# Kernel optimization log

Hardware: AMD Instinct MI355X
Metric: run time of the kernel (lower is better)

Reference implementation:

```python
import jax, jax.numpy as jnp
import numpy as np

H = 64  # LSTM hidden size ('unit' in the torch module)

def _lstm_params(k, scale):
    k1, k2, k3 = jax.random.split(k, 3)
    wih = jax.random.uniform(k1, (4 * H, 1), minval=-scale, maxval=scale, dtype=jnp.float32)
    whh = jax.random.uniform(k2, (4 * H, H), minval=-scale, maxval=scale, dtype=jnp.float32)
    b = jax.random.uniform(k3, (4 * H,), minval=-scale, maxval=scale, dtype=jnp.float32)  # b_ih + b_hh folded
    return wih, whh, b

def _linear_params(k, out_d, in_d):
    k1, k2 = jax.random.split(k)
    s = 1.0 / np.sqrt(in_d)
    w = jax.random.uniform(k1, (out_d, in_d), minval=-s, maxval=s, dtype=jnp.float32)
    b = jax.random.uniform(k2, (out_d,), minval=-s, maxval=s, dtype=jnp.float32)
    return w, b

def setup_inputs():
    key = jax.random.key(0)
    ks = jax.random.split(key, 16)
    B, T, A = 4096, 32, 6
    s = 1.0 / np.sqrt(H)
    inp = {
        'x0': jax.random.normal(ks[0], (B, T, 1), dtype=jnp.float32),
        'x1': jax.random.normal(ks[1], (B, T, 1), dtype=jnp.float32),
        'x2': jax.random.normal(ks[2], (B, T, 1), dtype=jnp.float32),
        's2': jax.random.normal(ks[3], (B, 3), dtype=jnp.float32),
    }
    for name, k in [('q00', ks[4]), ('q01', ks[5]), ('i00', ks[6]), ('i01', ks[7]), ('i02', ks[8])]:
        wih, whh, b = _lstm_params(k, s)
        inp[name + '_wih'], inp[name + '_whh'], inp[name + '_b'] = wih, whh, b
    inp['q03_w'], inp['q03_b'] = _linear_params(ks[9], H, 3)
    inp['q1_w'], inp['q1_b'] = _linear_params(ks[10], H, 4 * H)
    inp['q2_w'], inp['q2_b'] = _linear_params(ks[11], A, H)
    inp['i03_w'], inp['i03_b'] = _linear_params(ks[12], H, 3)
    inp['i1_w'], inp['i1_b'] = _linear_params(ks[13], H, 4 * H)
    inp['i2_w'], inp['i2_b'] = _linear_params(ks[14], A, H)
    return inp

def _lstm_hn(x, wih, whh, b):
    # x: [B,T,1] -> final hidden state h_T: [B,H]. PyTorch gate order: i, f, g, o.
    B = x.shape[0]
    gx = jnp.einsum('bti,gi->btg', x, wih) + b        # [B,T,4H], input part precomputed
    gx = jnp.swapaxes(gx, 0, 1)                        # [T,B,4H]
    h0 = jnp.zeros((B, H), x.dtype)
    def step(carry, g):
        h, c = carry
        g = g + h @ whh.T
        i, f, gg, o = jnp.split(g, 4, axis=-1)
        c = jax.nn.sigmoid(f) * c + jax.nn.sigmoid(i) * jnp.tanh(gg)
        h = jax.nn.sigmoid(o) * jnp.tanh(c)
        return (h, c), None
    (h, _), _ = jax.lax.scan(step, (h0, h0), gx)
    return h

def reference(x0, x1, x2, s2,
              q00_wih, q00_whh, q00_b, q01_wih, q01_whh, q01_b,
              i00_wih, i00_whh, i00_b, i01_wih, i01_whh, i01_b, i02_wih, i02_whh, i02_b,
              q03_w, q03_b, q1_w, q1_b, q2_w, q2_b,
              i03_w, i03_b, i1_w, i1_b, i2_w, i2_b):
    # q branch (NOTE: original code applies q01 to BOTH x1 and x2 -- reproduced faithfully)
    hn0 = _lstm_hn(x0, q00_wih, q00_whh, q00_b)
    hn1 = _lstm_hn(x1, q01_wih, q01_whh, q01_b)
    hn2 = _lstm_hn(x2, q01_wih, q01_whh, q01_b)
    hn3 = jax.nn.relu(s2 @ q03_w.T + q03_b)
    hq = jnp.concatenate([hn0, hn1, hn2, hn3], axis=1)  # [B,4H]
    q = jax.nn.relu(hq @ q1_w.T + q1_b)
    # i branch
    hn0 = _lstm_hn(x0, i00_wih, i00_whh, i00_b)
    hn1 = _lstm_hn(x1, i01_wih, i01_whh, i01_b)
    hn2 = _lstm_hn(x2, i02_wih, i02_whh, i02_b)
    hn3 = jax.nn.relu(s2 @ i03_w.T + i03_b)
    hi = jnp.concatenate([hn0, hn1, hn2, hn3], axis=1)
    i = jax.nn.relu(hi @ i1_w.T + i1_b)
    i = jax.nn.relu(i @ i2_w.T + i2_b)                   # [B,A]
    return (q @ q2_w.T + q2_b, jax.nn.log_softmax(i, axis=1), i)
```

## Files before the change

kernel.cpp:

```cpp
#include <hip/hip_runtime.h>

#define BTOT 4096
#define TS 32

typedef __attribute__((ext_vector_type(8))) short bfrag;
typedef __attribute__((ext_vector_type(4))) float f32x4;

#define S1 (-1.44269504089f)
#define S2 (-2.88539008178f)

__device__ __forceinline__ short f2bf(float f){
  union { float f; unsigned u; } v; v.f = f;
  unsigned r = v.u + 0x7FFFu + ((v.u >> 16) & 1u);
  return (short)(r >> 16);
}
__device__ __forceinline__ float bf2f(short s){
  union { unsigned u; float f; } v; v.u = ((unsigned)(unsigned short)s) << 16; return v.f;
}
__device__ __forceinline__ f32x4 exp2v(f32x4 a){
  f32x4 r;
  r[0] = __builtin_amdgcn_exp2f(a[0]);
  r[1] = __builtin_amdgcn_exp2f(a[1]);
  r[2] = __builtin_amdgcn_exp2f(a[2]);
  r[3] = __builtin_amdgcn_exp2f(a[3]);
  return r;
}
__device__ __forceinline__ f32x4 rcpv(f32x4 a){
  f32x4 r;
  r[0] = __builtin_amdgcn_rcpf(a[0]);
  r[1] = __builtin_amdgcn_rcpf(a[1]);
  r[2] = __builtin_amdgcn_rcpf(a[2]);
  r[3] = __builtin_amdgcn_rcpf(a[3]);
  return r;
}

struct LstmP {
  const float* x[6];
  const float* wih[6];
  const float* whh[6];
  const float* bias[6];
  float* hout;
};

struct EpiP {
  const float* hout;
  const float* s2;
  const float* w03[2]; const float* b03[2];
  const float* w1[2];  const float* b1[2];
  const float* w2[2];  const float* b2[2];
  float* out;
};

__global__ __launch_bounds__(256, 3) void lstm6(LstmP p){
  const int run = blockIdx.y;
  const int b0 = blockIdx.x * 32;
  const int t = threadIdx.x;
  const int w = t >> 6, lane = t & 63;
  const int i16 = lane & 15, q = lane >> 4;

  __shared__ bfrag hb[2][2][16*9];
  __shared__ float xsT[TS*36];

  const float* __restrict__ whh = p.whh[run];

  bfrag B[4][2];
  float wihv[4], bv[4];
#pragma unroll
  for (int g = 0; g < 4; ++g){
    const float sg = (g == 2) ? S2 : S1;
    const int n = 64*g + 16*w + i16;
    const float* wr = whh + n*64;
#pragma unroll
    for (int kf = 0; kf < 2; ++kf){
      const float* src = wr + 32*kf + 8*q;
      bfrag bb;
#pragma unroll
      for (int j = 0; j < 8; ++j) bb[j] = f2bf(src[j] * sg);
      B[g][kf] = bb;
    }
    wihv[g] = p.wih[run][n] * sg;
    bv[g]   = p.bias[run][n] * sg;
  }
  {
    const float* x = p.x[run] + (size_t)b0 * TS;
    for (int i = t; i < 32*TS; i += 256){
      int m = i >> 5, s = i & 31;
      xsT[s*36 + m] = x[i];
    }
    int* hz = (int*)&hb[0][0][0];
    for (int i = t; i < 1152; i += 256) hz[i] = 0;
  }
  __syncthreads();

  f32x4 c4[2];
  c4[0] = (f32x4){0.f,0.f,0.f,0.f};
  c4[1] = (f32x4){0.f,0.f,0.f,0.f};

  const int af = i16*9 + q;
  for (int s = 0; s < TS; ++s){
#pragma unroll
    for (int tile = 0; tile < 2; ++tile){
      const bfrag* hh = hb[s & 1][tile];
      short* wh = (short*)hb[(s+1) & 1][tile];
      bfrag ah0 = hh[af];
      bfrag ah1 = hh[af + 4];
      f32x4 xm4 = *(const f32x4*)(xsT + s*36 + 16*tile + 4*q);

      f32x4 acc[4];
#pragma unroll
      for (int g = 0; g < 4; ++g){
        acc[g] = xm4 * wihv[g] + bv[g];
        acc[g] = __builtin_amdgcn_mfma_f32_16x16x32_bf16(ah0, B[g][0], acc[g], 0,0,0);
        acc[g] = __builtin_amdgcn_mfma_f32_16x16x32_bf16(ah1, B[g][1], acc[g], 0,0,0);
      }
      f32x4 ei = exp2v(acc[0]);
      f32x4 ef = exp2v(acc[1]);
      f32x4 eg = exp2v(acc[2]);
      f32x4 eo = exp2v(acc[3]);
      f32x4 pf = 1.0f + ef;
      f32x4 D1 = (1.0f + eg) * (1.0f + ei);
      f32x4 num = __builtin_elementwise_fma(c4[tile], D1, (1.0f - eg) * pf);
      f32x4 cc = num * rcpv(pf * D1);
      c4[tile] = cc;
      f32x4 ec = exp2v(cc * S2);
      f32x4 hv = (1.0f - ec) * rcpv((1.0f + ec) * (1.0f + eo));
      if (s == TS-1){
#pragma unroll
        for (int r = 0; r < 4; ++r)
          p.hout[((size_t)run*BTOT + b0 + 16*tile + 4*q + r)*64 + 16*w + i16] = hv[r];
      } else {
        const int wbase = (4*q)*72 + 16*w + i16;
#pragma unroll
        for (int r = 0; r < 4; ++r)
          wh[wbase + r*72] = f2bf(hv[r]);
      }
    }
    __syncthreads();
  }
}

__global__ __launch_bounds__(256) void epilogue(EpiP p){
  const int br = blockIdx.y;
  const int b0 = blockIdx.x * 16;
  const int t = threadIdx.x;
  const int wave = t >> 6, lane = t & 63;
  const int i16 = lane & 15, q = lane >> 4;

  __shared__ bfrag hqv_hi[16*33], hqv_lo[16*33];
  __shared__ float qv[16*66];
  __shared__ float iv[16][6];

  const float* hbase = p.hout + (size_t)br*3*BTOT*64;
  {
    short4* dh = (short4*)hqv_hi;
    short4* dl = (short4*)hqv_lo;
    for (int i = t; i < 768; i += 256){
      int run = i >> 8, ii = i & 255;
      int e = ii >> 4, j4 = ii & 15;
      float4 v = *(const float4*)(hbase + ((size_t)run*BTOT + b0 + e)*64 + j4*4);
      short4 h, l;
      short x0 = f2bf(v.x); h.x = x0; l.x = f2bf(v.x - bf2f(x0));
      short x1 = f2bf(v.y); h.y = x1; l.y = f2bf(v.y - bf2f(x1));
      short x2 = f2bf(v.z); h.z = x2; l.z = f2bf(v.z - bf2f(x2));
      short x3 = f2bf(v.w); h.w = x3; l.w = f2bf(v.w - bf2f(x3));
      int o4 = e*66 + run*16 + j4;
      dh[o4] = h;
      dl[o4] = l;
    }
  }
  {
    short* sh = (short*)hqv_hi;
    short* sl = (short*)hqv_lo;
    const float* w03 = p.w03[br];
    const float* b03 = p.b03[br];
    for (int i = t; i < 1024; i += 256){
      int e = i >> 6, jj = i & 63;
      const float* s2r = p.s2 + (size_t)(b0 + e)*3;
      float v = fmaf(s2r[0], w03[jj*3+0],
                fmaf(s2r[1], w03[jj*3+1],
                fmaf(s2r[2], w03[jj*3+2], b03[jj])));
      v = fmaxf(v, 0.0f);
      int off = e*264 + 192 + jj;
      short hi = f2bf(v);
      sh[off] = hi;
      sl[off] = f2bf(v - bf2f(hi));
    }
  }
  __syncthreads();

  {
    const int n = 16*wave + i16;
    const float* w1r = p.w1[br] + (size_t)n*256;
    f32x4 acc;
    { float bb = p.b1[br][n]; acc[0]=bb; acc[1]=bb; acc[2]=bb; acc[3]=bb; }
#pragma unroll
    for (int ks = 0; ks < 8; ++ks){
      bfrag ah = hqv_hi[i16*33 + 4*ks + q];
      bfrag al = hqv_lo[i16*33 + 4*ks + q];
      const float* src = w1r + 32*ks + 8*q;
      bfrag bh, bl;
#pragma unroll
      for (int j = 0; j < 8; ++j){
        float f = src[j];
        short hi = f2bf(f);
        bh[j] = hi;
        bl[j] = f2bf(f - bf2f(hi));
      }
      acc = __builtin_amdgcn_mfma_f32_16x16x32_bf16(ah, bh, acc, 0,0,0);
      acc = __builtin_amdgcn_mfma_f32_16x16x32_bf16(al, bh, acc, 0,0,0);
      acc = __builtin_amdgcn_mfma_f32_16x16x32_bf16(ah, bl, acc, 0,0,0);
    }
#pragma unroll
    for (int r = 0; r < 4; ++r)
      qv[(4*q + r)*66 + n] = fmaxf(acc[r], 0.0f);
  }
  __syncthreads();

  if (t < 96){
    int e = t / 6, a = t % 6;
    const float* w2r = p.w2[br] + a*64;
    const float* qe = qv + e*66;
    float acc2 = p.b2[br][a];
#pragma unroll 8
    for (int k = 0; k < 64; ++k) acc2 = fmaf(qe[k], w2r[k], acc2);
    int b = b0 + e;
    if (br == 0){
      p.out[(size_t)b*6 + a] = acc2;
    } else {
      float v = fmaxf(acc2, 0.0f);
      iv[e][a] = v;
      p.out[(size_t)2*BTOT*6 + (size_t)b*6 + a] = v;
    }
  }
  __syncthreads();
  if (br == 1 && t < 16){
    float m = iv[t][0];
    for (int a2 = 1; a2 < 6; ++a2) m = fmaxf(m, iv[t][a2]);
    float ss = 0.0f;
    for (int a2 = 0; a2 < 6; ++a2) ss += __expf(iv[t][a2] - m);
    float ls = __logf(ss);
    int b = b0 + t;
    for (int a2 = 0; a2 < 6; ++a2)
      p.out[(size_t)BTOT*6 + (size_t)b*6 + a2] = iv[t][a2] - m - ls;
  }
}

extern "C" void kernel_launch(void* const* d_in, const int* in_sizes, int n_in,
                              void* d_out, int out_size, void* d_ws, size_t ws_size,
                              hipStream_t stream) {
  const float* x0 = (const float*)d_in[0];
  const float* x1 = (const float*)d_in[1];
  const float* x2 = (const float*)d_in[2];
  const float* s2 = (const float*)d_in[3];

  LstmP lp;
  lp.x[0]=x0; lp.x[1]=x1; lp.x[2]=x2; lp.x[3]=x0; lp.x[4]=x1; lp.x[5]=x2;
  const int wbase[6] = {4, 7, 7, 10, 13, 16};
  for (int r = 0; r < 6; ++r){
    lp.wih[r]  = (const float*)d_in[wbase[r]+0];
    lp.whh[r]  = (const float*)d_in[wbase[r]+1];
    lp.bias[r] = (const float*)d_in[wbase[r]+2];
  }
  lp.hout = (float*)d_ws;

  lstm6<<<dim3(BTOT/32, 6), 256, 0, stream>>>(lp);

  EpiP ep;
  ep.hout = (const float*)d_ws;
  ep.s2 = s2;
  ep.w03[0]=(const float*)d_in[19]; ep.b03[0]=(const float*)d_in[20];
  ep.w1 [0]=(const float*)d_in[21]; ep.b1 [0]=(const float*)d_in[22];
  ep.w2 [0]=(const float*)d_in[23]; ep.b2 [0]=(const float*)d_in[24];
  ep.w03[1]=(const float*)d_in[25]; ep.b03[1]=(const float*)d_in[26];
  ep.w1 [1]=(const float*)d_in[27]; ep.b1 [1]=(const float*)d_in[28];
  ep.w2 [1]=(const float*)d_in[29]; ep.b2 [1]=(const float*)d_in[30];
  ep.out = (float*)d_out;

  epilogue<<<dim3(BTOT/16, 2), 256, 0, stream>>>(ep);
}
```

Baseline: 184.5 us.

## Repartition LSTM blocks to two runs per block with 16-row batch tiles

Each block now processes two LSTM runs over 16 batch rows instead of one run over 32 rows. Each wave owns 32 hidden columns (two column groups) rather than 16, so every wave holds twice the recurrent weight fragments in registers. Input weights and biases move from registers into shared memory. The grid changes from 128x6 to 256x3 blocks, giving more independent blocks with shorter per-block work. In exchange, register pressure rises from the doubled B fragments, which may hurt occupancy under launch_bounds(256,3).

```diff
diff --git a/kernel.cpp b/kernel.cpp
--- a/kernel.cpp
+++ b/kernel.cpp
@@ -52,45 +52,61 @@
 };
 
 __global__ __launch_bounds__(256, 3) void lstm6(LstmP p){
-  const int run = blockIdx.y;
-  const int b0 = blockIdx.x * 32;
+  const int z = blockIdx.y;
+  const int b0 = blockIdx.x * 16;
   const int t = threadIdx.x;
-  const int w = t >> 6, lane = t & 63;
+  const int ww = t >> 6, lane = t & 63;
+  const int rl = ww >> 1, half = ww & 1;
+  const int run = 2*z + rl;
   const int i16 = lane & 15, q = lane >> 4;
 
   __shared__ bfrag hb[2][2][16*9];
-  __shared__ float xsT[TS*36];
+  __shared__ float xsT[2][TS*20];
+  __shared__ __align__(16) float wb[4][16][20];
 
   const float* __restrict__ whh = p.whh[run];
 
-  bfrag B[4][2];
-  float wihv[4], bv[4];
+  bfrag B[4][2][2];
 #pragma unroll
   for (int g = 0; g < 4; ++g){
     const float sg = (g == 2) ? S2 : S1;
-    const int n = 64*g + 16*w + i16;
-    const float* wr = whh + n*64;
-#pragma unroll
-    for (int kf = 0; kf < 2; ++kf){
-      const float* src = wr + 32*kf + 8*q;
-      bfrag bb;
-#pragma unroll
-      for (int j = 0; j < 8; ++j) bb[j] = f2bf(src[j] * sg);
-      B[g][kf] = bb;
-    }
-    wihv[g] = p.wih[run][n] * sg;
-    bv[g]   = p.bias[run][n] * sg;
-  }
-  {
+#pragma unroll
+    for (int cg = 0; cg < 2; ++cg){
+      const int n = 64*g + 32*half + 16*cg + i16;
+      const float* wr = whh + n*64;
+#pragma unroll
+      for (int kf = 0; kf < 2; ++kf){
+        const float* src = wr + 32*kf + 8*q;
+        bfrag bb;
+#pragma unroll
+        for (int j = 0; j < 8; ++j) bb[j] = f2bf(src[j] * sg);
+        B[g][cg][kf] = bb;
+      }
+      if (q == 0){
+        wb[ww][i16][cg*8 + g]     = p.wih[run][n] * sg;
+        wb[ww][i16][cg*8 + 4 + g] = p.bias[run][n] * sg;
+      }
+    }
+  }
+
+  if (half == 0){
     const float* x = p.x[run] + (size_t)b0 * TS;
-    for (int i = t; i < 32*TS; i += 256){
+    for (int i = lane; i < 16*TS; i += 64){
       int m = i >> 5, s = i & 31;
-      xsT[s*36 + m] = x[i];
-    }
+      xsT[rl][s*20 + m] = x[i];
+    }
+  }
+  {
     int* hz = (int*)&hb[0][0][0];
-    for (int i = t; i < 1152; i += 256) hz[i] = 0;
-  }
-  __syncthreads();
+    for (int i = t; i < 1152; i += 256){
+      int lr = i / 576, rem = i - lr*576;
+      hz[lr*1152 + rem] = 0;
+    }
+  }
+  __syncthreads();
+
+  const float* xp = xsT[rl];
+  const float* wbp = &wb[ww][i16][0];
 
   f32x4 c4[2];
   c4[0] = (f32x4){0.f,0.f,0.f,0.f};
@@ -98,20 +114,22 @@
 
   const int af = i16*9 + q;
   for (int s = 0; s < TS; ++s){
-#pragma unroll
-    for (int tile = 0; tile < 2; ++tile){
-      const bfrag* hh = hb[s & 1][tile];
-      short* wh = (short*)hb[(s+1) & 1][tile];
-      bfrag ah0 = hh[af];
-      bfrag ah1 = hh[af + 4];
-      f32x4 xm4 = *(const f32x4*)(xsT + s*36 + 16*tile + 4*q);
-
+    const bfrag* hh = hb[rl][s & 1];
+    short* wh = (short*)&hb[rl][(s+1) & 1][0];
+    bfrag ah0 = hh[af];
+    bfrag ah1 = hh[af + 4];
+    f32x4 xm4 = *(const f32x4*)(xp + s*20 + 4*q);
+
+#pragma unroll
+    for (int cg = 0; cg < 2; ++cg){
+      f32x4 wv = *(const f32x4*)(wbp + cg*8);
+      f32x4 bb = *(const f32x4*)(wbp + cg*8 + 4);
       f32x4 acc[4];
 #pragma unroll
       for (int g = 0; g < 4; ++g){
-        acc[g] = xm4 * wihv[g] + bv[g];
-        acc[g] = __builtin_amdgcn_mfma_f32_16x16x32_bf16(ah0, B[g][0], acc[g], 0,0,0);
-        acc[g] = __builtin_amdgcn_mfma_f32_16x16x32_bf16(ah1, B[g][1], acc[g], 0,0,0);
+        acc[g] = xm4 * wv[g] + bb[g];
+        acc[g] = __builtin_amdgcn_mfma_f32_16x16x32_bf16(ah0, B[g][cg][0], acc[g], 0,0,0);
+        acc[g] = __builtin_amdgcn_mfma_f32_16x16x32_bf16(ah1, B[g][cg][1], acc[g], 0,0,0);
       }
       f32x4 ei = exp2v(acc[0]);
       f32x4 ef = exp2v(acc[1]);
@@ -119,20 +137,20 @@
       f32x4 eo = exp2v(acc[3]);
       f32x4 pf = 1.0f + ef;
       f32x4 D1 = (1.0f + eg) * (1.0f + ei);
-      f32x4 num = __builtin_elementwise_fma(c4[tile], D1, (1.0f - eg) * pf);
+      f32x4 num = __builtin_elementwise_fma(c4[cg], D1, (1.0f - eg) * pf);
       f32x4 cc = num * rcpv(pf * D1);
-      c4[tile] = cc;
+      c4[cg] = cc;
       f32x4 ec = exp2v(cc * S2);
       f32x4 hv = (1.0f - ec) * rcpv((1.0f + ec) * (1.0f + eo));
       if (s == TS-1){
 #pragma unroll
-        for (int r = 0; r < 4; ++r)
-          p.hout[((size_t)run*BTOT + b0 + 16*tile + 4*q + r)*64 + 16*w + i16] = hv[r];
+        for (int rr = 0; rr < 4; ++rr)
+          p.hout[((size_t)run*BTOT + b0 + 4*q + rr)*64 + 32*half + 16*cg + i16] = hv[rr];
       } else {
-        const int wbase = (4*q)*72 + 16*w + i16;
-#pragma unroll
-        for (int r = 0; r < 4; ++r)
-          wh[wbase + r*72] = f2bf(hv[r]);
+        const int wbase = (4*q)*72 + 32*half + 16*cg + i16;
+#pragma unroll
+        for (int rr = 0; rr < 4; ++rr)
+          wh[wbase + rr*72] = f2bf(hv[rr]);
       }
     }
     __syncthreads();
@@ -263,7 +281,7 @@
   }
   lp.hout = (float*)d_ws;
 
-  lstm6<<<dim3(BTOT/32, 6), 256, 0, stream>>>(lp);
+  lstm6<<<dim3(BTOT/16, 3), 256, 0, stream>>>(lp);
 
   EpiP ep;
   ep.hout = (const float*)d_ws;
```

Measured after the change: 190.7 us. 3.4% more time.
